# Kernel tuning notes

Hardware: AMD Instinct MI355X
Metric: run time of the kernel (lower is better)

The kernel has to match this reference:

```python
import jax, jax.numpy as jnp
import numpy as np

B, L, D = 4, 1024, 1536
OUT = 9 + 7 * 2  # 23
TRANS_SCALE = 10.0
LN_EPS = 1e-5
NORM_EPS = 1e-5   # eps added to vector norms before divide in forward
GS_EPS = 1e-12    # eps inside Gram-Schmidt (RotationMatrix.from_graham_schmidt)

BB_COORDS = jnp.array([[-0.525, 1.363, 0.0],   # N
                       [0.0,    0.0,   0.0],   # CA
                       [1.526,  0.0,   0.0]],  # C
                      dtype=jnp.float32)


def _graham_schmidt(x_axis, xy_plane):
    # Returns rotation with columns [e0, e1, e2], shape [..., 3, 3]
    e0 = x_axis / jnp.sqrt((x_axis ** 2).sum(-1, keepdims=True) + GS_EPS)
    e1 = xy_plane - e0 * (e0 * xy_plane).sum(-1, keepdims=True)
    e1 = e1 / jnp.sqrt((e1 ** 2).sum(-1, keepdims=True) + GS_EPS)
    e2 = jnp.cross(e0, e1)
    return jnp.stack([e0, e1, e2], axis=-1)


def setup_inputs() -> dict:
    key = jax.random.key(0)
    ks = jax.random.split(key, 8)
    x = jax.random.normal(ks[0], (B, L, D), dtype=jnp.float32)
    # Build a valid prior affine (random rotation via Gram-Schmidt + random translation)
    v1 = jax.random.normal(ks[1], (B, L, 3), dtype=jnp.float32)
    v2 = jax.random.normal(ks[2], (B, L, 3), dtype=jnp.float32)
    R0 = _graham_schmidt(v1, v2)                       # [B, L, 3, 3]
    t0 = jax.random.normal(ks[3], (B, L, 3), dtype=jnp.float32) * 5.0
    affine = jnp.concatenate([R0.reshape(B, L, 9), t0], axis=-1)  # [B, L, 12]
    affine_mask = jax.random.uniform(ks[4], (B, L)) > 0.1
    w1 = jax.random.normal(ks[5], (D, D), dtype=jnp.float32) * 0.02
    b1 = jnp.zeros((D,), dtype=jnp.float32)
    ln_g = jnp.ones((D,), dtype=jnp.float32)
    ln_b = jnp.zeros((D,), dtype=jnp.float32)
    w2 = jax.random.normal(ks[6], (OUT, D), dtype=jnp.float32) * 0.02
    b2 = jnp.zeros((OUT,), dtype=jnp.float32)
    return {"x": x, "affine": affine, "affine_mask": affine_mask,
            "w1": w1, "b1": b1, "ln_g": ln_g, "ln_b": ln_b, "w2": w2, "b2": b2}


def reference(x, affine, affine_mask, w1, b1, ln_g, ln_b, w2, b2):
    # ffn1 -> GELU (exact/erf, matching nn.GELU()) -> LayerNorm -> proj
    h = jnp.einsum('bld,ed->ble', x, w1) + b1
    h = jax.nn.gelu(h, approximate=False)
    mu = h.mean(-1, keepdims=True)
    var = ((h - mu) ** 2).mean(-1, keepdims=True)
    h = (h - mu) / jnp.sqrt(var + LN_EPS) * ln_g + ln_b
    p = jnp.einsum('bld,od->blo', h, w2) + b2          # [B, L, 23]

    trans = p[..., 0:3] * TRANS_SCALE
    xv = p[..., 3:6]
    yv = p[..., 6:9]
    # angles = p[..., 9:23] split but unused in the returned values
    xv = xv / (jnp.linalg.norm(xv, axis=-1, keepdims=True) + NORM_EPS)
    yv = yv / (jnp.linalg.norm(yv, axis=-1, keepdims=True) + NORM_EPS)

    # Affine3D.from_graham_schmidt(x+trans, trans, y+trans):
    #   x_axis = origin - neg_x_axis, xy_plane = p_xy_plane - origin
    neg_x = xv + trans
    p_xy = yv + trans
    Ru = _graham_schmidt(trans - neg_x, p_xy - trans)  # [B, L, 3, 3]
    tu = trans

    # update.mask(affine_mask): identity where mask is False
    m = affine_mask[..., None]
    Ru = jnp.where(m[..., None], Ru, jnp.eye(3, dtype=x.dtype))
    tu = jnp.where(m, tu, jnp.zeros((), dtype=x.dtype))

    # compose prior rigid with update: R = R0 @ Ru, t = R0 @ tu + t0
    R0 = affine[..., :9].reshape(affine.shape[:-1] + (3, 3))
    t0 = affine[..., 9:]
    R = jnp.einsum('blij,bljk->blik', R0, Ru)
    t = jnp.einsum('blij,blj->bli', R0, tu) + t0

    affine_out = jnp.concatenate([R.reshape(R.shape[:-2] + (9,)), t], axis=-1)
    # apply rigid to the 3 local backbone atoms: [B, L, 3(atoms), 3(xyz)]
    pred_xyz = jnp.einsum('blij,aj->blai', R, BB_COORDS.astype(x.dtype)) + t[..., None, :]
    return affine_out, pred_xyz
```

## Files before the change

### kernel.cpp

```cpp
#include <hip/hip_runtime.h>
#include <hip/hip_bf16.h>
#include <math.h>

typedef __bf16 bf16x8 __attribute__((ext_vector_type(8)));
typedef float floatx4 __attribute__((ext_vector_type(4)));

#define DK    1536
#define MROWS 4096
#define NOUT  1536
#define OUTC  23
#define AFF_SZ (MROWS * 12)
#define HSTRIDE 1544

__device__ __forceinline__ unsigned int pkbf(float lo, float hi) {
    unsigned int a = __float_as_uint(lo) + 0x8000u;
    unsigned int b = __float_as_uint(hi) + 0x8000u;
    return (b & 0xffff0000u) | (a >> 16);
}
__device__ __forceinline__ unsigned short f2bf1(float v) {
    return (unsigned short)((__float_as_uint(v) + 0x8000u) >> 16);
}
__device__ __forceinline__ float bflo(unsigned int u) {
    return __uint_as_float(u << 16);
}
__device__ __forceinline__ float bfhi(unsigned int u) {
    return __uint_as_float(u & 0xffff0000u);
}

__global__ __launch_bounds__(256, 2)
void gemm1_kernel(const float* __restrict__ A, const float* __restrict__ Bm,
                  const float* __restrict__ b1, unsigned short* __restrict__ Hb)
{
    __shared__ __align__(16) unsigned short As[128][72];
    __shared__ __align__(16) unsigned short Bs[128][72];

    const int tid    = threadIdx.x;
    const int wave   = tid >> 6;
    const int lane   = tid & 63;
    const int wm     = (wave & 1) * 64;
    const int wn     = (wave >> 1) * 64;
    const int lane15 = lane & 15;
    const int quad   = lane >> 4;

    const int row0 = blockIdx.x * 128;
    const int col0 = blockIdx.y * 128;

    const int rbase = tid >> 4;
    const int c4    = (tid & 15) << 2;

    const float* Ab = A  + (size_t)(row0 + rbase) * DK + c4;
    const float* Bb = Bm + (size_t)(col0 + rbase) * DK + c4;

    floatx4 acc[4][4] = {};
    float4 pa[8], pb[8];

    #pragma unroll
    for (int i = 0; i < 8; ++i) {
        pa[i] = *(const float4*)(Ab + (size_t)(16 * i) * DK);
        pb[i] = *(const float4*)(Bb + (size_t)(16 * i) * DK);
    }

    for (int k0 = 0; k0 < DK; k0 += 64) {
        #pragma unroll
        for (int i = 0; i < 8; ++i) {
            unsigned int lo = pkbf(pa[i].x, pa[i].y);
            unsigned int hi = pkbf(pa[i].z, pa[i].w);
            *(uint2*)(&As[rbase + 16 * i][c4]) = make_uint2(lo, hi);
            lo = pkbf(pb[i].x, pb[i].y);
            hi = pkbf(pb[i].z, pb[i].w);
            *(uint2*)(&Bs[rbase + 16 * i][c4]) = make_uint2(lo, hi);
        }
        if (k0 + 64 < DK) {
            #pragma unroll
            for (int i = 0; i < 8; ++i) {
                pa[i] = *(const float4*)(Ab + (size_t)(16 * i) * DK + k0 + 64);
                pb[i] = *(const float4*)(Bb + (size_t)(16 * i) * DK + k0 + 64);
            }
        }
        __syncthreads();

        #pragma unroll
        for (int ks = 0; ks < 2; ++ks) {
            bf16x8 af[4], bfr[4];
            #pragma unroll
            for (int mt = 0; mt < 4; ++mt)
                af[mt] = *(const bf16x8*)(&As[wm + mt * 16 + lane15][ks * 32 + quad * 8]);
            #pragma unroll
            for (int nt = 0; nt < 4; ++nt)
                bfr[nt] = *(const bf16x8*)(&Bs[wn + nt * 16 + lane15][ks * 32 + quad * 8]);
            #pragma unroll
            for (int mt = 0; mt < 4; ++mt)
                #pragma unroll
                for (int nt = 0; nt < 4; ++nt)
                    acc[mt][nt] = __builtin_amdgcn_mfma_f32_16x16x32_bf16(
                        af[mt], bfr[nt], acc[mt][nt], 0, 0, 0);
        }
        __syncthreads();
    }

    #pragma unroll
    for (int mt = 0; mt < 4; ++mt)
        #pragma unroll
        for (int nt = 0; nt < 4; ++nt)
            #pragma unroll
            for (int r = 0; r < 4; ++r) {
                int row = row0 + wm + mt * 16 + quad * 4 + r;
                int col = col0 + wn + nt * 16 + lane15;
                float v = acc[mt][nt][r] + b1[col];
                v = 0.5f * v * (1.0f + erff(v * 0.70710678118654752f));
                Hb[(size_t)row * NOUT + col] = f2bf1(v);
            }
}

__global__ __launch_bounds__(256)
void head_kernel(const unsigned short* __restrict__ Hb, const float* __restrict__ ln_g,
                 const float* __restrict__ ln_b, const float* __restrict__ w2,
                 const float* __restrict__ b2, const float* __restrict__ affine,
                 const int* __restrict__ amask, float* __restrict__ out)
{
    __shared__ __align__(16) unsigned short hb[8][HSTRIDE];
    __shared__ float st[8][2];
    __shared__ float pred[2][16][17];
    __shared__ float pr[8][32];

    const int tid    = threadIdx.x;
    const int lane   = tid & 63;
    const int wave   = tid >> 6;
    const int lane15 = lane & 15;
    const int quad   = lane >> 4;
    const int row8   = blockIdx.x * 8;

    #pragma unroll
    for (int rr = 0; rr < 2; ++rr) {
        const int r = wave * 2 + rr;
        const unsigned short* src = Hb + (size_t)(row8 + r) * DK;
        float s = 0.f, ss = 0.f;
        #pragma unroll
        for (int j = 0; j < 3; ++j) {
            const int e8 = lane + 64 * j;
            uint4 u = *(const uint4*)(src + e8 * 8);
            *(uint4*)(&hb[r][e8 * 8]) = u;
            float f0 = bflo(u.x), f1 = bfhi(u.x), f2 = bflo(u.y), f3 = bfhi(u.y);
            float f4 = bflo(u.z), f5 = bfhi(u.z), f6 = bflo(u.w), f7 = bfhi(u.w);
            s  += ((f0 + f1) + (f2 + f3)) + ((f4 + f5) + (f6 + f7));
            ss += ((f0*f0 + f1*f1) + (f2*f2 + f3*f3)) + ((f4*f4 + f5*f5) + (f6*f6 + f7*f7));
        }
        #pragma unroll
        for (int off = 32; off > 0; off >>= 1) {
            s  += __shfl_down(s, off, 64);
            ss += __shfl_down(ss, off, 64);
        }
        if (lane == 0) {
            float mu  = s * (1.f / DK);
            float var = ss * (1.f / DK) - mu * mu;
            st[r][0] = mu;
            st[r][1] = 1.f / sqrtf(var + 1e-5f);
        }
    }
    __syncthreads();

    {
        const int r   = tid >> 5;
        const int c32 = tid & 31;
        const float mu = st[r][0], rstd = st[r][1];
        const float murstd = mu * rstd;
        #pragma unroll
        for (int jj = 0; jj < 6; ++jj) {
            const int e8 = c32 + 32 * jj;
            const int d  = e8 * 8;
            uint4 u = *(uint4*)(&hb[r][d]);
            float4 g0 = *(const float4*)(ln_g + d);
            float4 g1 = *(const float4*)(ln_g + d + 4);
            float4 b0 = *(const float4*)(ln_b + d);
            float4 b1v = *(const float4*)(ln_b + d + 4);
            float h0 = fmaf(bflo(u.x), rstd, -murstd), h1 = fmaf(bfhi(u.x), rstd, -murstd);
            float h2 = fmaf(bflo(u.y), rstd, -murstd), h3 = fmaf(bfhi(u.y), rstd, -murstd);
            float h4 = fmaf(bflo(u.z), rstd, -murstd), h5 = fmaf(bfhi(u.z), rstd, -murstd);
            float h6 = fmaf(bflo(u.w), rstd, -murstd), h7 = fmaf(bfhi(u.w), rstd, -murstd);
            h0 = fmaf(h0, g0.x, b0.x);  h1 = fmaf(h1, g0.y, b0.y);
            h2 = fmaf(h2, g0.z, b0.z);  h3 = fmaf(h3, g0.w, b0.w);
            h4 = fmaf(h4, g1.x, b1v.x); h5 = fmaf(h5, g1.y, b1v.y);
            h6 = fmaf(h6, g1.z, b1v.z); h7 = fmaf(h7, g1.w, b1v.w);
            u.x = pkbf(h0, h1); u.y = pkbf(h2, h3);
            u.z = pkbf(h4, h5); u.w = pkbf(h6, h7);
            *(uint4*)(&hb[r][d]) = u;
        }
    }
    __syncthreads();

    {
        const int ntile = wave & 1;
        const int khalf = wave >> 1;
        const int o     = ntile * 16 + lane15;
        const int osafe = (o < OUTC) ? o : 0;
        const float* wrow = w2 + (size_t)osafe * DK;
        const int mrow  = lane15 & 7;

        floatx4 acc = {0.f, 0.f, 0.f, 0.f};
        #pragma unroll 4
        for (int kk = 0; kk < 24; ++kk) {
            const int kb = khalf * 768 + kk * 32 + quad * 8;
            bf16x8 afr = *(const bf16x8*)(&hb[mrow][kb]);
            float4 wa = *(const float4*)(wrow + kb);
            float4 wb = *(const float4*)(wrow + kb + 4);
            union { unsigned int u[4]; bf16x8 v; } bu;
            bu.u[0] = pkbf(wa.x, wa.y);
            bu.u[1] = pkbf(wa.z, wa.w);
            bu.u[2] = pkbf(wb.x, wb.y);
            bu.u[3] = pkbf(wb.z, wb.w);
            acc = __builtin_amdgcn_mfma_f32_16x16x32_bf16(afr, bu.v, acc, 0, 0, 0);
        }

        if (khalf == 1) {
            #pragma unroll
            for (int r2 = 0; r2 < 4; ++r2)
                pred[ntile][quad * 4 + r2][lane15] = acc[r2];
        }
        __syncthreads();
        if (khalf == 0) {
            #pragma unroll
            for (int r2 = 0; r2 < 4; ++r2) {
                const int row = quad * 4 + r2;
                if (row < 8 && o < OUTC)
                    pr[row][o] = acc[r2] + pred[ntile][row][lane15] + b2[o];
            }
        }
    }
    __syncthreads();

    if (tid < 8) {
        const int row = row8 + tid;
        float p[OUTC];
        #pragma unroll
        for (int oo = 0; oo < OUTC; ++oo) p[oo] = pr[tid][oo];

        float trans[3] = { p[0] * 10.f, p[1] * 10.f, p[2] * 10.f };
        float xv[3] = { p[3], p[4], p[5] };
        float yv[3] = { p[6], p[7], p[8] };
        float xn = sqrtf(xv[0]*xv[0] + xv[1]*xv[1] + xv[2]*xv[2]) + 1e-5f;
        xv[0] /= xn; xv[1] /= xn; xv[2] /= xn;
        float yn = sqrtf(yv[0]*yv[0] + yv[1]*yv[1] + yv[2]*yv[2]) + 1e-5f;
        yv[0] /= yn; yv[1] /= yn; yv[2] /= yn;

        float a0 = -xv[0], a1 = -xv[1], a2 = -xv[2];
        float inv = 1.f / sqrtf(a0*a0 + a1*a1 + a2*a2 + 1e-12f);
        float e0x = a0 * inv, e0y = a1 * inv, e0z = a2 * inv;
        float c = e0x*yv[0] + e0y*yv[1] + e0z*yv[2];
        float e1x = yv[0] - e0x * c, e1y = yv[1] - e0y * c, e1z = yv[2] - e0z * c;
        inv = 1.f / sqrtf(e1x*e1x + e1y*e1y + e1z*e1z + 1e-12f);
        e1x *= inv; e1y *= inv; e1z *= inv;
        float e2x = e0y*e1z - e0z*e1y;
        float e2y = e0z*e1x - e0x*e1z;
        float e2z = e0x*e1y - e0y*e1x;

        float Ru[3][3] = { { e0x, e1x, e2x },
                           { e0y, e1y, e2y },
                           { e0z, e1z, e2z } };
        float tu[3] = { trans[0], trans[1], trans[2] };
        if (amask[row] == 0) {
            Ru[0][0]=1.f; Ru[0][1]=0.f; Ru[0][2]=0.f;
            Ru[1][0]=0.f; Ru[1][1]=1.f; Ru[1][2]=0.f;
            Ru[2][0]=0.f; Ru[2][1]=0.f; Ru[2][2]=1.f;
            tu[0]=tu[1]=tu[2]=0.f;
        }

        const float* af = affine + (size_t)row * 12;
        float R0[3][3] = { { af[0], af[1], af[2] },
                           { af[3], af[4], af[5] },
                           { af[6], af[7], af[8] } };
        float t0[3] = { af[9], af[10], af[11] };

        float R[3][3], t[3];
        #pragma unroll
        for (int i = 0; i < 3; ++i) {
            #pragma unroll
            for (int j = 0; j < 3; ++j)
                R[i][j] = R0[i][0]*Ru[0][j] + R0[i][1]*Ru[1][j] + R0[i][2]*Ru[2][j];
            t[i] = R0[i][0]*tu[0] + R0[i][1]*tu[1] + R0[i][2]*tu[2] + t0[i];
        }

        float* oa = out + (size_t)row * 12;
        #pragma unroll
        for (int i = 0; i < 3; ++i) {
            #pragma unroll
            for (int j = 0; j < 3; ++j) oa[i*3 + j] = R[i][j];
            oa[9 + i] = t[i];
        }

        const float BB[3][3] = { { -0.525f, 1.363f, 0.f },
                                 {  0.f,    0.f,   0.f },
                                 {  1.526f, 0.f,   0.f } };
        float* op = out + AFF_SZ + (size_t)row * 9;
        #pragma unroll
        for (int a = 0; a < 3; ++a)
            #pragma unroll
            for (int i = 0; i < 3; ++i)
                op[a*3 + i] = R[i][0]*BB[a][0] + R[i][1]*BB[a][1] + R[i][2]*BB[a][2] + t[i];
    }
}

extern "C" void kernel_launch(void* const* d_in, const int* in_sizes, int n_in,
                              void* d_out, int out_size, void* d_ws, size_t ws_size,
                              hipStream_t stream) {
    const float* x      = (const float*)d_in[0];
    const float* affine = (const float*)d_in[1];
    const int*   amask  = (const int*)  d_in[2];
    const float* w1     = (const float*)d_in[3];
    const float* b1     = (const float*)d_in[4];
    const float* ln_g   = (const float*)d_in[5];
    const float* ln_b   = (const float*)d_in[6];
    const float* w2     = (const float*)d_in[7];
    const float* b2     = (const float*)d_in[8];
    float* out = (float*)d_out;
    unsigned short* Hb = (unsigned short*)d_ws;

    dim3 g1(MROWS / 128, NOUT / 128);
    gemm1_kernel<<<g1, 256, 0, stream>>>(x, w1, b1, Hb);
    head_kernel<<<MROWS / 8, 256, 0, stream>>>(Hb, ln_g, ln_b, w2, b2, affine, amask, out);
}
```

Measured before the change: 149.0 us.

## Pre-convert weights to bf16, fold LayerNorm into head projection, shrink GEMM tile

Adds a setup kernel that converts w1 to bf16 once and builds a gamma-scaled bf16 copy of w2 plus per-output constants, so the LayerNorm affine and mean subtraction fold algebraically into the projection epilogue. The head kernel no longer normalizes H in shared memory; it runs MFMA directly on raw H and applies rstd*(S - mu*c1) + c2 afterward. The main GEMM uses 64-row tiles with more blocks and higher occupancy, loading bf16 weights directly instead of converting per tile. It adds an extra launch and a full pass over w1 every call, and bf16 rounding of gamma*w2 may shift numerics slightly.

```diff
diff --git a/kernel.cpp b/kernel.cpp
--- a/kernel.cpp
+++ b/kernel.cpp
@@ -10,7 +10,10 @@
 #define NOUT  1536
 #define OUTC  23
 #define AFF_SZ (MROWS * 12)
-#define HSTRIDE 1544
+
+#define W1B_OFF 12582912
+#define WP_OFF  17301504
+#define C_OFF   17399808
 
 __device__ __forceinline__ unsigned int pkbf(float lo, float hi) {
     unsigned int a = __float_as_uint(lo) + 0x8000u;
@@ -20,76 +23,130 @@
 __device__ __forceinline__ unsigned short f2bf1(float v) {
     return (unsigned short)((__float_as_uint(v) + 0x8000u) >> 16);
 }
-__device__ __forceinline__ float bflo(unsigned int u) {
-    return __uint_as_float(u << 16);
-}
-__device__ __forceinline__ float bfhi(unsigned int u) {
-    return __uint_as_float(u & 0xffff0000u);
-}
-
-__global__ __launch_bounds__(256, 2)
-void gemm1_kernel(const float* __restrict__ A, const float* __restrict__ Bm,
+__device__ __forceinline__ float bflo(unsigned int u) { return __uint_as_float(u << 16); }
+__device__ __forceinline__ float bfhi(unsigned int u) { return __uint_as_float(u & 0xffff0000u); }
+
+__global__ __launch_bounds__(256)
+void setup_kernel(const float* __restrict__ w1, const float* __restrict__ ln_g,
+                  const float* __restrict__ ln_b, const float* __restrict__ w2,
+                  unsigned short* __restrict__ w1b, unsigned short* __restrict__ wpb,
+                  float* __restrict__ c12)
+{
+    const int b = blockIdx.x, tid = threadIdx.x;
+    if (b < 1152) {
+        const int base = b * 2048 + tid * 8;
+        float4 a = *(const float4*)(w1 + base);
+        float4 c = *(const float4*)(w1 + base + 4);
+        uint4 u;
+        u.x = pkbf(a.x, a.y); u.y = pkbf(a.z, a.w);
+        u.z = pkbf(c.x, c.y); u.w = pkbf(c.z, c.w);
+        *(uint4*)(w1b + base) = u;
+    } else if (b < 1176) {
+        const int base = (b - 1152) * 2048 + tid * 8;
+        const int o = base / DK;
+        const int d = base - o * DK;
+        uint4 u = make_uint4(0, 0, 0, 0);
+        if (o < OUTC) {
+            float4 a  = *(const float4*)(w2 + (size_t)o * DK + d);
+            float4 c  = *(const float4*)(w2 + (size_t)o * DK + d + 4);
+            float4 g0 = *(const float4*)(ln_g + d);
+            float4 g1 = *(const float4*)(ln_g + d + 4);
+            u.x = pkbf(a.x * g0.x, a.y * g0.y);
+            u.y = pkbf(a.z * g0.z, a.w * g0.w);
+            u.z = pkbf(c.x * g1.x, c.y * g1.y);
+            u.w = pkbf(c.z * g1.z, c.w * g1.w);
+        }
+        *(uint4*)(wpb + base) = u;
+    } else {
+        const int o = b - 1176;
+        float s1 = 0.f, s2 = 0.f;
+        for (int d = tid; d < DK; d += 256) {
+            float w = w2[(size_t)o * DK + d];
+            s1 += ln_g[d] * w;
+            s2 += ln_b[d] * w;
+        }
+        __shared__ float r1[4], r2[4];
+        const int lane = tid & 63, wave = tid >> 6;
+        #pragma unroll
+        for (int off = 32; off > 0; off >>= 1) {
+            s1 += __shfl_down(s1, off, 64);
+            s2 += __shfl_down(s2, off, 64);
+        }
+        if (lane == 0) { r1[wave] = s1; r2[wave] = s2; }
+        __syncthreads();
+        if (tid == 0) {
+            c12[o]      = r1[0] + r1[1] + r1[2] + r1[3];
+            c12[32 + o] = r2[0] + r2[1] + r2[2] + r2[3];
+        }
+    }
+}
+
+__global__ __launch_bounds__(256, 4)
+void gemm1_kernel(const float* __restrict__ A, const unsigned short* __restrict__ Bw,
                   const float* __restrict__ b1, unsigned short* __restrict__ Hb)
 {
-    __shared__ __align__(16) unsigned short As[128][72];
+    __shared__ __align__(16) unsigned short As[64][72];
     __shared__ __align__(16) unsigned short Bs[128][72];
 
     const int tid    = threadIdx.x;
     const int wave   = tid >> 6;
     const int lane   = tid & 63;
-    const int wm     = (wave & 1) * 64;
+    const int wm     = (wave & 1) * 32;
     const int wn     = (wave >> 1) * 64;
     const int lane15 = lane & 15;
     const int quad   = lane >> 4;
 
-    const int row0 = blockIdx.x * 128;
+    const int row0 = blockIdx.x * 64;
     const int col0 = blockIdx.y * 128;
 
-    const int rbase = tid >> 4;
-    const int c4    = (tid & 15) << 2;
-
-    const float* Ab = A  + (size_t)(row0 + rbase) * DK + c4;
-    const float* Bb = Bm + (size_t)(col0 + rbase) * DK + c4;
-
-    floatx4 acc[4][4] = {};
-    float4 pa[8], pb[8];
+    const int arow = tid >> 4;
+    const int ac4  = (tid & 15) << 2;
+    const int brow = tid >> 3;
+    const int b8   = (tid & 7) << 3;
+
+    const float*          Ap = A  + (size_t)(row0 + arow) * DK + ac4;
+    const unsigned short* Bp = Bw + (size_t)(col0 + brow) * DK + b8;
+
+    floatx4 acc[2][4] = {};
+    float4 pa[4];
+    uint4  pb[4];
 
     #pragma unroll
-    for (int i = 0; i < 8; ++i) {
-        pa[i] = *(const float4*)(Ab + (size_t)(16 * i) * DK);
-        pb[i] = *(const float4*)(Bb + (size_t)(16 * i) * DK);
-    }
+    for (int i = 0; i < 4; ++i) pa[i] = *(const float4*)(Ap + (size_t)(16 * i) * DK);
+    #pragma unroll
+    for (int i = 0; i < 4; ++i) pb[i] = *(const uint4*)(Bp + (size_t)(32 * i) * DK);
 
     for (int k0 = 0; k0 < DK; k0 += 64) {
         #pragma unroll
-        for (int i = 0; i < 8; ++i) {
-            unsigned int lo = pkbf(pa[i].x, pa[i].y);
-            unsigned int hi = pkbf(pa[i].z, pa[i].w);
-            *(uint2*)(&As[rbase + 16 * i][c4]) = make_uint2(lo, hi);
-            lo = pkbf(pb[i].x, pb[i].y);
-            hi = pkbf(pb[i].z, pb[i].w);
-            *(uint2*)(&Bs[rbase + 16 * i][c4]) = make_uint2(lo, hi);
-        }
+        for (int i = 0; i < 4; ++i) {
+            uint2 u = make_uint2(pkbf(pa[i].x, pa[i].y), pkbf(pa[i].z, pa[i].w));
+            *(uint2*)(&As[arow + 16 * i][ac4]) = u;
+        }
+        #pragma unroll
+        for (int i = 0; i < 4; ++i)
+            *(uint4*)(&Bs[brow + 32 * i][b8]) = pb[i];
+
         if (k0 + 64 < DK) {
             #pragma unroll
-            for (int i = 0; i < 8; ++i) {
-                pa[i] = *(const float4*)(Ab + (size_t)(16 * i) * DK + k0 + 64);
-                pb[i] = *(const float4*)(Bb + (size_t)(16 * i) * DK + k0 + 64);
-            }
+            for (int i = 0; i < 4; ++i)
+                pa[i] = *(const float4*)(Ap + (size_t)(16 * i) * DK + k0 + 64);
+            #pragma unroll
+            for (int i = 0; i < 4; ++i)
+                pb[i] = *(const uint4*)(Bp + (size_t)(32 * i) * DK + k0 + 64);
         }
         __syncthreads();
 
         #pragma unroll
         for (int ks = 0; ks < 2; ++ks) {
-            bf16x8 af[4], bfr[4];
-            #pragma unroll
-            for (int mt = 0; mt < 4; ++mt)
+            bf16x8 af[2], bfr[4];
+            #pragma unroll
+            for (int mt = 0; mt < 2; ++mt)
                 af[mt] = *(const bf16x8*)(&As[wm + mt * 16 + lane15][ks * 32 + quad * 8]);
             #pragma unroll
             for (int nt = 0; nt < 4; ++nt)
                 bfr[nt] = *(const bf16x8*)(&Bs[wn + nt * 16 + lane15][ks * 32 + quad * 8]);
             #pragma unroll
-            for (int mt = 0; mt < 4; ++mt)
+            for (int mt = 0; mt < 2; ++mt)
                 #pragma unroll
                 for (int nt = 0; nt < 4; ++nt)
                     acc[mt][nt] = __builtin_amdgcn_mfma_f32_16x16x32_bf16(
@@ -99,7 +156,7 @@
     }
 
     #pragma unroll
-    for (int mt = 0; mt < 4; ++mt)
+    for (int mt = 0; mt < 2; ++mt)
         #pragma unroll
         for (int nt = 0; nt < 4; ++nt)
             #pragma unroll
@@ -113,14 +170,14 @@
 }
 
 __global__ __launch_bounds__(256)
-void head_kernel(const unsigned short* __restrict__ Hb, const float* __restrict__ ln_g,
-                 const float* __restrict__ ln_b, const float* __restrict__ w2,
-                 const float* __restrict__ b2, const float* __restrict__ affine,
-                 const int* __restrict__ amask, float* __restrict__ out)
+void head_kernel(const unsigned short* __restrict__ Hb, const unsigned short* __restrict__ Wp,
+                 const float* __restrict__ c12, const float* __restrict__ b2,
+                 const float* __restrict__ affine, const int* __restrict__ amask,
+                 float* __restrict__ out)
 {
-    __shared__ __align__(16) unsigned short hb[8][HSTRIDE];
+    __shared__ __align__(16) unsigned short hb[8][DK];
     __shared__ float st[8][2];
-    __shared__ float pred[2][16][17];
+    __shared__ float pred[4][16][32];
     __shared__ float pr[8][32];
 
     const int tid    = threadIdx.x;
@@ -160,70 +217,34 @@
     __syncthreads();
 
     {
-        const int r   = tid >> 5;
-        const int c32 = tid & 31;
-        const float mu = st[r][0], rstd = st[r][1];
-        const float murstd = mu * rstd;
-        #pragma unroll
-        for (int jj = 0; jj < 6; ++jj) {
-            const int e8 = c32 + 32 * jj;
-            const int d  = e8 * 8;
-            uint4 u = *(uint4*)(&hb[r][d]);
-            float4 g0 = *(const float4*)(ln_g + d);
-            float4 g1 = *(const float4*)(ln_g + d + 4);
-            float4 b0 = *(const float4*)(ln_b + d);
-            float4 b1v = *(const float4*)(ln_b + d + 4);
-            float h0 = fmaf(bflo(u.x), rstd, -murstd), h1 = fmaf(bfhi(u.x), rstd, -murstd);
-            float h2 = fmaf(bflo(u.y), rstd, -murstd), h3 = fmaf(bfhi(u.y), rstd, -murstd);
-            float h4 = fmaf(bflo(u.z), rstd, -murstd), h5 = fmaf(bfhi(u.z), rstd, -murstd);
-            float h6 = fmaf(bflo(u.w), rstd, -murstd), h7 = fmaf(bfhi(u.w), rstd, -murstd);
-            h0 = fmaf(h0, g0.x, b0.x);  h1 = fmaf(h1, g0.y, b0.y);
-            h2 = fmaf(h2, g0.z, b0.z);  h3 = fmaf(h3, g0.w, b0.w);
-            h4 = fmaf(h4, g1.x, b1v.x); h5 = fmaf(h5, g1.y, b1v.y);
-            h6 = fmaf(h6, g1.z, b1v.z); h7 = fmaf(h7, g1.w, b1v.w);
-            u.x = pkbf(h0, h1); u.y = pkbf(h2, h3);
-            u.z = pkbf(h4, h5); u.w = pkbf(h6, h7);
-            *(uint4*)(&hb[r][d]) = u;
+        const int mrow = lane15 & 7;
+        const unsigned short* w0  = Wp + (size_t)lane15 * DK;
+        const unsigned short* w1r = Wp + (size_t)(16 + lane15) * DK;
+        floatx4 a0 = {0.f, 0.f, 0.f, 0.f}, a1 = {0.f, 0.f, 0.f, 0.f};
+        #pragma unroll
+        for (int kk = 0; kk < 12; ++kk) {
+            const int kb = wave * 384 + kk * 32 + quad * 8;
+            bf16x8 afr = *(const bf16x8*)(&hb[mrow][kb]);
+            bf16x8 bf0 = *(const bf16x8*)(w0 + kb);
+            bf16x8 bf1 = *(const bf16x8*)(w1r + kb);
+            a0 = __builtin_amdgcn_mfma_f32_16x16x32_bf16(afr, bf0, a0, 0, 0, 0);
+            a1 = __builtin_amdgcn_mfma_f32_16x16x32_bf16(afr, bf1, a1, 0, 0, 0);
+        }
+        #pragma unroll
+        for (int r2 = 0; r2 < 4; ++r2) {
+            pred[wave][quad * 4 + r2][lane15]      = a0[r2];
+            pred[wave][quad * 4 + r2][16 + lane15] = a1[r2];
         }
     }
     __syncthreads();
 
     {
-        const int ntile = wave & 1;
-        const int khalf = wave >> 1;
-        const int o     = ntile * 16 + lane15;
-        const int osafe = (o < OUTC) ? o : 0;
-        const float* wrow = w2 + (size_t)osafe * DK;
-        const int mrow  = lane15 & 7;
-
-        floatx4 acc = {0.f, 0.f, 0.f, 0.f};
-        #pragma unroll 4
-        for (int kk = 0; kk < 24; ++kk) {
-            const int kb = khalf * 768 + kk * 32 + quad * 8;
-            bf16x8 afr = *(const bf16x8*)(&hb[mrow][kb]);
-            float4 wa = *(const float4*)(wrow + kb);
-            float4 wb = *(const float4*)(wrow + kb + 4);
-            union { unsigned int u[4]; bf16x8 v; } bu;
-            bu.u[0] = pkbf(wa.x, wa.y);
-            bu.u[1] = pkbf(wa.z, wa.w);
-            bu.u[2] = pkbf(wb.x, wb.y);
-            bu.u[3] = pkbf(wb.z, wb.w);
-            acc = __builtin_amdgcn_mfma_f32_16x16x32_bf16(afr, bu.v, acc, 0, 0, 0);
-        }
-
-        if (khalf == 1) {
-            #pragma unroll
-            for (int r2 = 0; r2 < 4; ++r2)
-                pred[ntile][quad * 4 + r2][lane15] = acc[r2];
-        }
-        __syncthreads();
-        if (khalf == 0) {
-            #pragma unroll
-            for (int r2 = 0; r2 < 4; ++r2) {
-                const int row = quad * 4 + r2;
-                if (row < 8 && o < OUTC)
-                    pr[row][o] = acc[r2] + pred[ntile][row][lane15] + b2[o];
-            }
+        const int row = tid >> 5;
+        const int o   = tid & 31;
+        if (o < OUTC) {
+            float S = pred[0][row][o] + pred[1][row][o] + pred[2][row][o] + pred[3][row][o];
+            float mu = st[row][0], rstd = st[row][1];
+            pr[row][o] = rstd * (S - mu * c12[o]) + c12[32 + o] + b2[o];
         }
     }
     __syncthreads();
@@ -312,9 +333,15 @@
     const float* w2     = (const float*)d_in[7];
     const float* b2     = (const float*)d_in[8];
     float* out = (float*)d_out;
-    unsigned short* Hb = (unsigned short*)d_ws;
-
-    dim3 g1(MROWS / 128, NOUT / 128);
-    gemm1_kernel<<<g1, 256, 0, stream>>>(x, w1, b1, Hb);
-    head_kernel<<<MROWS / 8, 256, 0, stream>>>(Hb, ln_g, ln_b, w2, b2, affine, amask, out);
-}
+
+    unsigned char* ws = (unsigned char*)d_ws;
+    unsigned short* Hb  = (unsigned short*)(ws);
+    unsigned short* w1b = (unsigned short*)(ws + W1B_OFF);
+    unsigned short* Wp  = (unsigned short*)(ws + WP_OFF);
+    float*          c12 = (float*)(ws + C_OFF);
+
+    setup_kernel<<<1152 + 24 + OUTC, 256, 0, stream>>>(w1, ln_g, ln_b, w2, w1b, Wp, c12);
+    dim3 g1(MROWS / 64, NOUT / 128);
+    gemm1_kernel<<<g1, 256, 0, stream>>>(x, w1b, b1, Hb);
+    head_kernel<<<MROWS / 8, 256, 0, stream>>>(Hb, Wp, c12, b2, affine, amask, out);
+}
```

After: 196.6 us. 31.9% more time.
